# Optimization experiments

Measured on AMD Instinct MI355X. Metric: run time of the kernel, lower is better.

Reference implementation:

```python
import jax, jax.numpy as jnp
import numpy as np

B = 8192   # batch of trajectories
T = 32     # time points
H = 256    # hidden_dim
NL = 4     # num_layers
EPS = 1e-5 # LayerNorm eps (torch default)


def setup_inputs() -> dict:
    key = jax.random.key(0)
    ks = jax.random.split(key, 8)
    # xavier-ish scales (gain 0.5 for hidden, 0.1 for output, per _init_weights)
    s0 = 0.5 * np.sqrt(2.0 / (6 + H))
    sh = 0.5 * np.sqrt(2.0 / (H + H))
    so = 0.1 * np.sqrt(2.0 / (H + 3))
    return {
        "y0": jax.random.normal(ks[0], (B, 3), dtype=jnp.float32),
        "t_span": jnp.arange(T, dtype=jnp.float32) * 0.01,
        "params": jax.random.uniform(ks[1], (B, 3), dtype=jnp.float32),  # [Omega, Delta, gamma] > 0
        "W0": jax.random.normal(ks[2], (6, H), dtype=jnp.float32) * s0,
        "b0": jnp.zeros((H,), dtype=jnp.float32),
        "Wh": jax.random.normal(ks[3], (NL - 1, H, H), dtype=jnp.float32) * sh,
        "bh": jnp.zeros((NL - 1, H), dtype=jnp.float32),
        "ln_g": jnp.ones((NL, H), dtype=jnp.float32),
        "ln_b": jnp.zeros((NL, H), dtype=jnp.float32),
        "Wout": jax.random.normal(ks[4], (H, 3), dtype=jnp.float32) * so,
        "bout": jnp.zeros((3,), dtype=jnp.float32),
        "gate": jnp.float32(0.5),
    }


def _layernorm(h, g, b):
    mu = jnp.mean(h, axis=-1, keepdims=True)
    var = jnp.mean(jnp.square(h - mu), axis=-1, keepdims=True)
    return (h - mu) * jax.lax.rsqrt(var + EPS) * g + b


def reference(y0, t_span, params, W0, b0, Wh, bh, ln_g, ln_b, Wout, bout, gate):
    def correction_net(y, p):
        # input: concat([u,v,w, Omega,Delta,gamma]) -> (B, 6)
        h = jnp.concatenate([y, p], axis=-1) @ W0 + b0
        h = jax.nn.silu(_layernorm(h, ln_g[0], ln_b[0]))
        for i in range(NL - 1):
            h = jax.nn.silu(_layernorm(h @ Wh[i] + bh[i], ln_g[i + 1], ln_b[i + 1]))
        return h @ Wout + bout  # (B, 3)

    def bloch_rhs_incomplete(y, p):
        u, v, w = y[:, 0:1], y[:, 1:2], y[:, 2:3]
        Om, ga = p[:, 0:1], p[:, 2:3]
        du = -ga * u
        dv = -ga * v - Om * w
        dw = -2.0 * ga * (w + 1.0) + Om * v
        return jnp.concatenate([du, dv, dw], axis=-1)

    def f_total(y):
        return bloch_rhs_incomplete(y, params) + gate * correction_net(y, params)

    def rk4_step(y, dt):
        k1 = f_total(y)
        k2 = f_total(y + 0.5 * dt * k1)
        k3 = f_total(y + 0.5 * dt * k2)
        k4 = f_total(y + dt * k3)
        y_new = y + (dt / 6.0) * (k1 + 2.0 * k2 + 2.0 * k3 + k4)
        return y_new, y_new

    dts = jnp.diff(t_span)              # (T-1,)
    _, ys = jax.lax.scan(rk4_step, y0, dts)
    return jnp.concatenate([y0[None], ys], axis=0)  # (T, B, 3)
```

## Files before the change

kernel.cpp:

```cpp
#include <hip/hip_runtime.h>

typedef unsigned short u16;
typedef short v8s   __attribute__((ext_vector_type(8)));
typedef float f32x4 __attribute__((ext_vector_type(4)));
typedef float f32x2 __attribute__((ext_vector_type(2)));

#define H_ 256
#define B_ 8192
#define NSTEP 31
#define NTHREADS 512
#define NBLOCKS 256
#define AROW 264

#define MFMA16(a,b,c) __builtin_amdgcn_mfma_f32_16x16x32_bf16(a,b,c,0,0,0)

#define DPP_QP_XOR1 0xB1
#define DPP_QP_XOR2 0x4E
#define DPP_ROR4    0x124
#define DPP_ROR8    0x128

template<int CTRL>
__device__ __forceinline__ float dpp_add(float v){
  return v + __int_as_float(
      __builtin_amdgcn_update_dpp(0, __float_as_int(v), CTRL, 0xF, 0xF, true));
}

__device__ __forceinline__ u16 f2bf_rne(float f){
  unsigned u = __float_as_uint(f);
  u += 0x7fffu + ((u >> 16) & 1u);
  return (u16)(u >> 16);
}
__device__ __forceinline__ u16 f2bf_trunc(float f){
  return (u16)(__float_as_uint(f) >> 16);
}

#define WS_W0   0
#define WS_W1   8192
#define WS_W23  73728
#define WS_WO   204800
#define WS_TOT  205824

__global__ void prep_kernel(const float* __restrict__ W0,
                            const float* __restrict__ b0,
                            const float* __restrict__ Wh,
                            const float* __restrict__ Wout,
                            u16* __restrict__ ws){
  int i = blockIdx.x * 256 + threadIdx.x;
  if (i < 8192){
    int q = i >> 11, n = (i >> 3) & 255, j = i & 7;
    int k = q*8 + j;
    float v = (k < 6) ? W0[k*H_ + n] : ((k == 6) ? b0[n] : 0.f);
    ws[i] = f2bf_rne(v);
  } else if (i < 73728){
    int r = i - 8192;
    int n = r >> 8, k = r & 255;
    ws[i] = f2bf_rne(Wh[k*H_ + n]);
  } else if (i < 204800){
    int r = i - 73728;
    int l = r >> 16, r2 = r & 65535;
    int kc = r2 >> 13, r3 = r2 & 8191;
    int q = r3 >> 11, n = (r3 >> 3) & 255, j = r3 & 7;
    int k = kc*32 + q*8 + j;
    ws[i] = f2bf_rne(Wh[(1 + l)*H_*H_ + k*H_ + n]);
  } else if (i < WS_TOT){
    int r = i - 204800;
    int kc = r >> 7, q = (r >> 5) & 3, nn = (r >> 3) & 3, j = r & 7;
    int k = kc*32 + q*8 + j;
    ws[i] = f2bf_rne(nn < 3 ? Wout[k*3 + nn] : 0.f);
  }
}

#define PWROW 10
#define OFF_A      0
#define OFF_W1     16896
#define OFF_WOUT   152064
#define OFF_PART   154112
#define OFF_MR     156672
#define OFF_NET    156928
#define OFF_YCUR   157440
#define OFF_YSUM   157952
#define OFF_YSTG   158464
#define OFF_P      158976
#define OFF_DTS    159488
#define LDS_TOTAL  159616

__global__ __launch_bounds__(NTHREADS, 2)
void pinode_kernel(const float* __restrict__ y0g, const float* __restrict__ t_span,
                   const float* __restrict__ params, const float* __restrict__ bhg,
                   const float* __restrict__ ln_gg, const float* __restrict__ ln_bg,
                   const float* __restrict__ boutg, const float* __restrict__ gatep,
                   const u16* __restrict__ ws, float* __restrict__ out)
{
  extern __shared__ char smem[];
  u16*   A    = (u16*)(smem + OFF_A);
  u16*   W1   = (u16*)(smem + OFF_W1);
  u16*   WO   = (u16*)(smem + OFF_WOUT);
  float* part = (float*)(smem + OFF_PART);
  float* mrs  = (float*)(smem + OFF_MR);
  float* net  = (float*)(smem + OFF_NET);
  float* ycur = (float*)(smem + OFF_YCUR);
  float* ysum = (float*)(smem + OFF_YSUM);
  float* ystg = (float*)(smem + OFF_YSTG);
  float* pL   = (float*)(smem + OFF_P);
  float* dts  = (float*)(smem + OFF_DTS);

  const int tid = threadIdx.x;
  const int wave = tid >> 6;
  const int lane = tid & 63;
  const int q    = lane >> 4;
  const int c15  = lane & 15;
  const int colbase = wave * 32;
  const int s0 = blockIdx.x * 32;

  for (int idx = tid; idx < 8192; idx += NTHREADS){
    int n = idx >> 5, ch = idx & 31;
    *(v8s*)(W1 + n*AROW + ch*8) = *(const v8s*)(ws + WS_W1 + n*256 + ch*8);
  }
  if (tid < 128)
    *(v8s*)(WO + tid*8) = *(const v8s*)(ws + WS_WO + tid*8);
  if (tid < 96){
    int s = tid & 31, c = tid >> 5;
    float y = y0g[(s0+s)*3 + c];
    ycur[s*4+c] = y; ystg[s*4+c] = y;
    pL[s*4+c]   = params[(s0+s)*3 + c];
    out[(s0+s)*3 + c] = y;
  }
  if (tid < NSTEP) dts[tid] = t_span[tid+1] - t_span[tid];

  v8s wf[2][8][2];
#pragma unroll
  for (int l = 0; l < 2; ++l)
#pragma unroll
    for (int kc = 0; kc < 8; ++kc)
#pragma unroll
      for (int nt = 0; nt < 2; ++nt)
        wf[l][kc][nt] = *(const v8s*)(ws + WS_W23 +
            (((l*8 + kc)*4 + q)*256 + colbase + nt*16 + c15)*8);

  v8s w0f[2];
#pragma unroll
  for (int nt = 0; nt < 2; ++nt)
    w0f[nt] = *(const v8s*)(ws + WS_W0 + (q*256 + colbase + nt*16 + c15)*8);

  float lng[4][2], lnb[4][2], bia[4][2];
#pragma unroll
  for (int l = 0; l < 4; ++l)
#pragma unroll
    for (int nt = 0; nt < 2; ++nt){
      int col = colbase + nt*16 + c15;
      lng[l][nt] = ln_gg[l*H_ + col];
      lnb[l][nt] = ln_bg[l*H_ + col];
      bia[l][nt] = (l == 0) ? 0.f : bhg[(l-1)*H_ + col];
    }
  const float gate = gatep[0];
  const float bo0 = boutg[0], bo1 = boutg[1], bo2 = boutg[2];
  const f32x4 fzero = {0.f, 0.f, 0.f, 0.f};

  const u16* pa  = A + c15*AROW + q*8;
  const u16* pw  = W1 + (colbase + c15)*AROW + q*8;
  u16* pstA = A + (q*4)*AROW + colbase + c15;

  __syncthreads();

  {
    int s = tid >> 4, pr = tid & 15;
    int e0 = pr*2, e1 = e0 + 1;
    float x0 = (e0 < 3) ? ystg[s*4+e0] : ((e0 < 6) ? pL[s*4+e0-3] : (e0 == 6 ? 1.f : 0.f));
    float x1 = (e1 < 3) ? ystg[s*4+e1] : ((e1 < 6) ? pL[s*4+e1-3] : (e1 == 6 ? 1.f : 0.f));
    unsigned pk = (unsigned)f2bf_rne(x0) | ((unsigned)f2bf_rne(x1) << 16);
    *(unsigned*)(A + s*AROW + e0) = pk;
  }
  __syncthreads();

  auto ln_silu = [&](f32x4 (&acc)[2][2], int li){
    float rs[2][4], rq[2][4];
#pragma unroll
    for (int mt = 0; mt < 2; ++mt)
#pragma unroll
      for (int r = 0; r < 4; ++r){
        float a0 = acc[mt][0][r], a1 = acc[mt][1][r];
        rs[mt][r] = a0 + a1;
        rq[mt][r] = a0*a0 + a1*a1;
      }
#pragma unroll
    for (int mt = 0; mt < 2; ++mt)
#pragma unroll
      for (int r = 0; r < 4; ++r){
        float s = rs[mt][r], qq = rq[mt][r];
        s = dpp_add<DPP_QP_XOR1>(s);  qq = dpp_add<DPP_QP_XOR1>(qq);
        s = dpp_add<DPP_QP_XOR2>(s);  qq = dpp_add<DPP_QP_XOR2>(qq);
        s = dpp_add<DPP_ROR4>(s);     qq = dpp_add<DPP_ROR4>(qq);
        s = dpp_add<DPP_ROR8>(s);     qq = dpp_add<DPP_ROR8>(qq);
        rs[mt][r] = s; rq[mt][r] = qq;
      }
    if (c15 == 0){
#pragma unroll
      for (int mt = 0; mt < 2; ++mt)
#pragma unroll
        for (int r = 0; r < 4; ++r){
          int row = mt*16 + q*4 + r;
          f32x2 v; v.x = rs[mt][r]; v.y = rq[mt][r];
          *(f32x2*)(part + (row*PWROW + wave)*2) = v;
        }
    }
    __syncthreads();
    if (tid < 32){
      const f32x4* pp = (const f32x4*)(part + tid*PWROW*2);
      f32x4 p0 = pp[0], p1 = pp[1], p2 = pp[2], p3 = pp[3];
      float S = p0[0]+p0[2]+p1[0]+p1[2]+p2[0]+p2[2]+p3[0]+p3[2];
      float Q = p0[1]+p0[3]+p1[1]+p1[3]+p2[1]+p2[3]+p3[1]+p3[3];
      float mean = S * (1.f/256.f);
      float var  = Q * (1.f/256.f) - mean*mean;
      float rstd = rsqrtf(var + 1e-5f);
      f32x2 mr; mr.x = rstd; mr.y = -mean*rstd;
      *(f32x2*)(mrs + tid*2) = mr;
    }
    __syncthreads();
#pragma unroll
    for (int mt = 0; mt < 2; ++mt)
#pragma unroll
      for (int r = 0; r < 4; ++r){
        int row = mt*16 + q*4 + r;
        f32x2 mr = *(const f32x2*)(mrs + row*2);
#pragma unroll
        for (int nt = 0; nt < 2; ++nt){
          float t  = acc[mt][nt][r] * mr.x + mr.y;
          float v  = t * lng[li][nt] + lnb[li][nt];
          float e  = __builtin_amdgcn_exp2f(v * -1.44269504f);
          float sv = v * __builtin_amdgcn_rcpf(1.f + e);
          pstA[(mt*16 + r)*AROW + nt*16] = f2bf_trunc(sv);
        }
      }
    __syncthreads();
  };

#pragma unroll 1
  for (int step = 0; step < NSTEP; ++step){
    float dt = dts[step];
#pragma unroll 1
    for (int stage = 0; stage < 4; ++stage){
      f32x4 acc[2][2];

#pragma unroll
      for (int mt = 0; mt < 2; ++mt)
#pragma unroll
        for (int nt = 0; nt < 2; ++nt) acc[mt][nt] = fzero;
      {
        v8s a0 = *(const v8s*)(pa);
        v8s a1 = *(const v8s*)(pa + 16*AROW);
        acc[0][0] = MFMA16(a0, w0f[0], acc[0][0]);
        acc[0][1] = MFMA16(a0, w0f[1], acc[0][1]);
        acc[1][0] = MFMA16(a1, w0f[0], acc[1][0]);
        acc[1][1] = MFMA16(a1, w0f[1], acc[1][1]);
      }
      ln_silu(acc, 0);

#pragma unroll
      for (int mt = 0; mt < 2; ++mt)
#pragma unroll
        for (int nt = 0; nt < 2; ++nt) acc[mt][nt] = fzero;
#pragma unroll
      for (int kc = 0; kc < 8; ++kc){
        v8s a0 = *(const v8s*)(pa + kc*32);
        v8s a1 = *(const v8s*)(pa + 16*AROW + kc*32);
        v8s bb0 = *(const v8s*)(pw + kc*32);
        v8s bb1 = *(const v8s*)(pw + 16*AROW + kc*32);
        acc[0][0] = MFMA16(a0, bb0, acc[0][0]);
        acc[0][1] = MFMA16(a0, bb1, acc[0][1]);
        acc[1][0] = MFMA16(a1, bb0, acc[1][0]);
        acc[1][1] = MFMA16(a1, bb1, acc[1][1]);
      }
#pragma unroll
      for (int mt = 0; mt < 2; ++mt)
#pragma unroll
        for (int nt = 0; nt < 2; ++nt)
#pragma unroll
          for (int r = 0; r < 4; ++r) acc[mt][nt][r] += bia[1][nt];
      ln_silu(acc, 1);

#pragma unroll
      for (int l = 0; l < 2; ++l){
#pragma unroll
        for (int mt = 0; mt < 2; ++mt)
#pragma unroll
          for (int nt = 0; nt < 2; ++nt) acc[mt][nt] = fzero;
#pragma unroll
        for (int kc = 0; kc < 8; ++kc){
          v8s a0 = *(const v8s*)(pa + kc*32);
          v8s a1 = *(const v8s*)(pa + 16*AROW + kc*32);
          acc[0][0] = MFMA16(a0, wf[l][kc][0], acc[0][0]);
          acc[0][1] = MFMA16(a0, wf[l][kc][1], acc[0][1]);
          acc[1][0] = MFMA16(a1, wf[l][kc][0], acc[1][0]);
          acc[1][1] = MFMA16(a1, wf[l][kc][1], acc[1][1]);
        }
#pragma unroll
        for (int mt = 0; mt < 2; ++mt)
#pragma unroll
          for (int nt = 0; nt < 2; ++nt)
#pragma unroll
            for (int r = 0; r < 4; ++r) acc[mt][nt][r] += bia[2+l][nt];
        ln_silu(acc, 2+l);
      }

      if (wave < 2){
        f32x4 ao = fzero;
        int nn = c15 < 3 ? c15 : 3;
#pragma unroll
        for (int kc = 0; kc < 8; ++kc){
          v8s a = *(const v8s*)(A + (wave*16 + c15)*AROW + kc*32 + q*8);
          v8s b = *(const v8s*)(WO + ((kc*4 + q)*4 + nn)*8);
          ao = MFMA16(a, b, ao);
        }
        if (c15 < 3){
#pragma unroll
          for (int r = 0; r < 4; ++r)
            net[(wave*16 + q*4 + r)*4 + c15] = ao[r];
        }
      }
      __syncthreads();

      if (tid < 32){
        int s = tid;
        float u = ystg[s*4+0], v = ystg[s*4+1], w = ystg[s*4+2];
        float Om = pL[s*4+0], ga = pL[s*4+2];
        float kk[3];
        kk[0] = -ga*u                      + gate*(net[s*4+0] + bo0);
        kk[1] = -ga*v - Om*w               + gate*(net[s*4+1] + bo1);
        kk[2] = -2.f*ga*(w + 1.f) + Om*v   + gate*(net[s*4+2] + bo2);
#pragma unroll
        for (int c = 0; c < 3; ++c){
          float yc = ycur[s*4+c];
          float k  = kk[c];
          float ys;
          if (stage == 3){
            float accw = ysum[s*4+c] + dt*(1.f/6.f)*k;
            ycur[s*4+c] = accw;
            ys = accw;
            out[(step+1)*(B_*3) + (s0+s)*3 + c] = accw;
          } else {
            float accw = (stage == 0) ? (yc + dt*(1.f/6.f)*k)
                                      : (ysum[s*4+c] + dt*(1.f/3.f)*k);
            ysum[s*4+c] = accw;
            ys = yc + ((stage == 2) ? dt : 0.5f*dt)*k;
          }
          ystg[s*4+c] = ys;
          A[s*AROW + c] = f2bf_rne(ys);
        }
      }
      __syncthreads();
    }
  }
}

extern "C" void kernel_launch(void* const* d_in, const int* in_sizes, int n_in,
                              void* d_out, int out_size, void* d_ws, size_t ws_size,
                              hipStream_t stream) {
  const float* y0     = (const float*)d_in[0];
  const float* t_span = (const float*)d_in[1];
  const float* params = (const float*)d_in[2];
  const float* W0     = (const float*)d_in[3];
  const float* b0     = (const float*)d_in[4];
  const float* Wh     = (const float*)d_in[5];
  const float* bh     = (const float*)d_in[6];
  const float* ln_g   = (const float*)d_in[7];
  const float* ln_b   = (const float*)d_in[8];
  const float* Wout   = (const float*)d_in[9];
  const float* bout   = (const float*)d_in[10];
  const float* gate   = (const float*)d_in[11];
  float* out = (float*)d_out;
  u16* ws = (u16*)d_ws;

  prep_kernel<<<WS_TOT/256, 256, 0, stream>>>(W0, b0, Wh, Wout, ws);

  hipFuncSetAttribute(reinterpret_cast<const void*>(pinode_kernel),
                      hipFuncAttributeMaxDynamicSharedMemorySize, LDS_TOTAL);
  pinode_kernel<<<NBLOCKS, NTHREADS, LDS_TOTAL, stream>>>(
      y0, t_span, params, bh, ln_g, ln_b, bout, gate, ws, out);
}
```

Baseline: 1.167 ms.

## Software-pipeline two 16-row groups through layers with atomic LayerNorm stats

Splits the 32-sample tile into two 16-row groups and interleaves them, so one group's matmul overlaps the other group's LayerNorm/SiLU. Row statistics are accumulated with LDS atomicAdd into double-buffered stat slots instead of per-wave partials plus a separate reduce pass. This cuts barriers per layer from three to one. The output projection and RK4 update are fused into per-wave work, removing the net buffer and the tid<32 serial stage. The cost is more atomics and more complex sequencing that depends on careful zeroing of the stat slots.

```diff
diff --git a/kernel.cpp b/kernel.cpp
--- a/kernel.cpp
+++ b/kernel.cpp
@@ -70,19 +70,16 @@
   }
 }
 
-#define PWROW 10
 #define OFF_A      0
 #define OFF_W1     16896
 #define OFF_WOUT   152064
-#define OFF_PART   154112
-#define OFF_MR     156672
-#define OFF_NET    156928
-#define OFF_YCUR   157440
-#define OFF_YSUM   157952
-#define OFF_YSTG   158464
-#define OFF_P      158976
-#define OFF_DTS    159488
-#define LDS_TOTAL  159616
+#define OFF_STAT   154112
+#define OFF_YCUR   154624
+#define OFF_YSUM   155136
+#define OFF_YSTG   155648
+#define OFF_P      156160
+#define OFF_DTS    156672
+#define LDS_TOTAL  156800
 
 __global__ __launch_bounds__(NTHREADS, 2)
 void pinode_kernel(const float* __restrict__ y0g, const float* __restrict__ t_span,
@@ -95,9 +92,7 @@
   u16*   A    = (u16*)(smem + OFF_A);
   u16*   W1   = (u16*)(smem + OFF_W1);
   u16*   WO   = (u16*)(smem + OFF_WOUT);
-  float* part = (float*)(smem + OFF_PART);
-  float* mrs  = (float*)(smem + OFF_MR);
-  float* net  = (float*)(smem + OFF_NET);
+  float* stat = (float*)(smem + OFF_STAT);
   float* ycur = (float*)(smem + OFF_YCUR);
   float* ysum = (float*)(smem + OFF_YSUM);
   float* ystg = (float*)(smem + OFF_YSTG);
@@ -109,6 +104,7 @@
   const int lane = tid & 63;
   const int q    = lane >> 4;
   const int c15  = lane & 15;
+  const int nn   = (c15 < 3) ? c15 : 3;
   const int colbase = wave * 32;
   const int s0 = blockIdx.x * 32;
 
@@ -126,6 +122,7 @@
     out[(s0+s)*3 + c] = y;
   }
   if (tid < NSTEP) dts[tid] = t_span[tid+1] - t_span[tid];
+  if (tid < 128) stat[tid] = 0.f;
 
   v8s wf[2][8][2];
 #pragma unroll
@@ -158,7 +155,6 @@
 
   const u16* pa  = A + c15*AROW + q*8;
   const u16* pw  = W1 + (colbase + c15)*AROW + q*8;
-  u16* pstA = A + (q*4)*AROW + colbase + c15;
 
   __syncthreads();
 
@@ -172,183 +168,182 @@
   }
   __syncthreads();
 
-  auto ln_silu = [&](f32x4 (&acc)[2][2], int li){
-    float rs[2][4], rq[2][4];
-#pragma unroll
-    for (int mt = 0; mt < 2; ++mt)
+
+  auto zstat = [&](int g, int par){
+    if (tid < 16)
+      *(f32x2*)(stat + ((g*2 + par)*16 + tid)*2) = (f32x2){0.f, 0.f};
+  };
+
+  auto mm0 = [&](f32x4 (&acc)[2], int g){
+    v8s a = *(const v8s*)(pa + g*16*AROW);
+    acc[0] = MFMA16(a, w0f[0], fzero);
+    acc[1] = MFMA16(a, w0f[1], fzero);
+  };
+
+  auto mm1 = [&](f32x4 (&acc)[2], int g){
+    float b0i = bia[1][0], b1i = bia[1][1];
+    acc[0] = (f32x4){b0i,b0i,b0i,b0i};
+    acc[1] = (f32x4){b1i,b1i,b1i,b1i};
+    const u16* pag = pa + g*16*AROW;
+#pragma unroll
+    for (int kc = 0; kc < 8; ++kc){
+      v8s a   = *(const v8s*)(pag + kc*32);
+      v8s bb0 = *(const v8s*)(pw + kc*32);
+      v8s bb1 = *(const v8s*)(pw + 16*AROW + kc*32);
+      acc[0] = MFMA16(a, bb0, acc[0]);
+      acc[1] = MFMA16(a, bb1, acc[1]);
+    }
+  };
+
+  auto mmr = [&](f32x4 (&acc)[2], int g, int lw){
+    float b0i = bia[2+lw][0], b1i = bia[2+lw][1];
+    acc[0] = (f32x4){b0i,b0i,b0i,b0i};
+    acc[1] = (f32x4){b1i,b1i,b1i,b1i};
+    const u16* pag = pa + g*16*AROW;
+#pragma unroll
+    for (int kc = 0; kc < 8; ++kc){
+      v8s a = *(const v8s*)(pag + kc*32);
+      acc[0] = MFMA16(a, wf[lw][kc][0], acc[0]);
+      acc[1] = MFMA16(a, wf[lw][kc][1], acc[1]);
+    }
+  };
+
+  auto red_write = [&](f32x4 (&acc)[2], int g, int par){
+    float rs[4], rq[4];
+#pragma unroll
+    for (int r = 0; r < 4; ++r){
+      float a0 = acc[0][r], a1 = acc[1][r];
+      rs[r] = a0 + a1;
+      rq[r] = a0*a0 + a1*a1;
+    }
+#pragma unroll
+    for (int r = 0; r < 4; ++r){
+      float s = rs[r], qq = rq[r];
+      s = dpp_add<DPP_QP_XOR1>(s);  qq = dpp_add<DPP_QP_XOR1>(qq);
+      s = dpp_add<DPP_QP_XOR2>(s);  qq = dpp_add<DPP_QP_XOR2>(qq);
+      s = dpp_add<DPP_ROR4>(s);     qq = dpp_add<DPP_ROR4>(qq);
+      s = dpp_add<DPP_ROR8>(s);     qq = dpp_add<DPP_ROR8>(qq);
+      rs[r] = s; rq[r] = qq;
+    }
+    if (c15 == 0){
+      float* bp = stat + ((g*2 + par)*16 + q*4)*2;
 #pragma unroll
       for (int r = 0; r < 4; ++r){
-        float a0 = acc[mt][0][r], a1 = acc[mt][1][r];
-        rs[mt][r] = a0 + a1;
-        rq[mt][r] = a0*a0 + a1*a1;
+        atomicAdd(bp + r*2 + 0, rs[r]);
+        atomicAdd(bp + r*2 + 1, rq[r]);
       }
-#pragma unroll
-    for (int mt = 0; mt < 2; ++mt)
+    }
+  };
+
+  auto finrm = [&](f32x4 (&acc)[2], int g, int li){
+    const int par = li & 1;
+    const float* bp = stat + ((g*2 + par)*16 + q*4)*2;
+    f32x4 st01 = *(const f32x4*)(bp);
+    f32x4 st23 = *(const f32x4*)(bp + 4);
+    float S[4] = {st01[0], st01[2], st23[0], st23[2]};
+    float Q[4] = {st01[1], st01[3], st23[1], st23[3]};
+    u16* pst = A + (g*16 + q*4)*AROW + colbase + c15;
+#pragma unroll
+    for (int r = 0; r < 4; ++r){
+      float mean = S[r] * (1.f/256.f);
+      float var  = Q[r] * (1.f/256.f) - mean*mean;
+      float rstd = rsqrtf(var + 1e-5f);
+      float mb   = -mean * rstd;
+#pragma unroll
+      for (int nt = 0; nt < 2; ++nt){
+        float t  = acc[nt][r] * rstd + mb;
+        float v  = t * lng[li][nt] + lnb[li][nt];
+        float e  = __builtin_amdgcn_exp2f(v * -1.44269504f);
+        float sv = v * __builtin_amdgcn_rcpf(1.f + e);
+        pst[r*AROW + nt*16] = f2bf_trunc(sv);
+      }
+    }
+  };
+
+  auto outrk4 = [&](int g, int step, int stage){
+    f32x4 ao = fzero;
+    const u16* pao = A + (g*16 + c15)*AROW + q*8;
+#pragma unroll
+    for (int kc = 0; kc < 8; ++kc){
+      v8s a = *(const v8s*)(pao + kc*32);
+      v8s b = *(const v8s*)(WO + ((kc*4 + q)*4 + nn)*8);
+      ao = MFMA16(a, b, ao);
+    }
+    float dt = dts[step];
+    if (c15 == 3){
 #pragma unroll
       for (int r = 0; r < 4; ++r){
-        float s = rs[mt][r], qq = rq[mt][r];
-        s = dpp_add<DPP_QP_XOR1>(s);  qq = dpp_add<DPP_QP_XOR1>(qq);
-        s = dpp_add<DPP_QP_XOR2>(s);  qq = dpp_add<DPP_QP_XOR2>(qq);
-        s = dpp_add<DPP_ROR4>(s);     qq = dpp_add<DPP_ROR4>(qq);
-        s = dpp_add<DPP_ROR8>(s);     qq = dpp_add<DPP_ROR8>(qq);
-        rs[mt][r] = s; rq[mt][r] = qq;
+        int s = g*16 + q*4 + r;
+        *(unsigned*)(A + s*AROW + 6) = 0x00003F80u;
       }
-    if (c15 == 0){
-#pragma unroll
-      for (int mt = 0; mt < 2; ++mt)
-#pragma unroll
-        for (int r = 0; r < 4; ++r){
-          int row = mt*16 + q*4 + r;
-          f32x2 v; v.x = rs[mt][r]; v.y = rq[mt][r];
-          *(f32x2*)(part + (row*PWROW + wave)*2) = v;
+    }
+    if (c15 < 3){
+      const int c = c15;
+      const float boc = (c == 0) ? bo0 : ((c == 1) ? bo1 : bo2);
+#pragma unroll
+      for (int r = 0; r < 4; ++r){
+        int s = g*16 + q*4 + r;
+        float Om = pL[s*4+0], ga = pL[s*4+2];
+        float yi  = ystg[s*4+c];
+        float oth = ystg[s*4 + ((c == 1) ? 2 : 1)];
+        float kA = (c == 2) ? (Om*oth - 2.f*ga*(yi + 1.f))
+                            : (-ga*yi - ((c == 1) ? Om*oth : 0.f));
+        float kk = kA + gate*(ao[r] + boc);
+        float yc = ycur[s*4+c];
+        if (stage == 3){
+          float acw = ysum[s*4+c] + dt*(1.f/6.f)*kk;
+          ycur[s*4+c] = acw;
+          ystg[s*4+c] = acw;
+          A[s*AROW + c] = f2bf_rne(acw);
+          out[(step+1)*(B_*3) + (s0+s)*3 + c] = acw;
+        } else {
+          float acw = (stage == 0) ? (yc + dt*(1.f/6.f)*kk)
+                                   : (ysum[s*4+c] + dt*(1.f/3.f)*kk);
+          ysum[s*4+c] = acw;
+          float ysn = yc + ((stage == 2) ? dt : 0.5f*dt)*kk;
+          ystg[s*4+c] = ysn;
+          A[s*AROW + c] = f2bf_rne(ysn);
         }
-    }
-    __syncthreads();
-    if (tid < 32){
-      const f32x4* pp = (const f32x4*)(part + tid*PWROW*2);
-      f32x4 p0 = pp[0], p1 = pp[1], p2 = pp[2], p3 = pp[3];
-      float S = p0[0]+p0[2]+p1[0]+p1[2]+p2[0]+p2[2]+p3[0]+p3[2];
-      float Q = p0[1]+p0[3]+p1[1]+p1[3]+p2[1]+p2[3]+p3[1]+p3[3];
-      float mean = S * (1.f/256.f);
-      float var  = Q * (1.f/256.f) - mean*mean;
-      float rstd = rsqrtf(var + 1e-5f);
-      f32x2 mr; mr.x = rstd; mr.y = -mean*rstd;
-      *(f32x2*)(mrs + tid*2) = mr;
-    }
-    __syncthreads();
-#pragma unroll
-    for (int mt = 0; mt < 2; ++mt)
-#pragma unroll
-      for (int r = 0; r < 4; ++r){
-        int row = mt*16 + q*4 + r;
-        f32x2 mr = *(const f32x2*)(mrs + row*2);
-#pragma unroll
-        for (int nt = 0; nt < 2; ++nt){
-          float t  = acc[mt][nt][r] * mr.x + mr.y;
-          float v  = t * lng[li][nt] + lnb[li][nt];
-          float e  = __builtin_amdgcn_exp2f(v * -1.44269504f);
-          float sv = v * __builtin_amdgcn_rcpf(1.f + e);
-          pstA[(mt*16 + r)*AROW + nt*16] = f2bf_trunc(sv);
-        }
+        A[s*AROW + 3 + c] = f2bf_rne(pL[s*4+c]);
       }
-    __syncthreads();
-  };
+    }
+  };
+
+  f32x4 accA[2], accB[2];
+
+  mm0(accA, 0); red_write(accA, 0, 0); zstat(0, 1);
+  __syncthreads();
 
 #pragma unroll 1
-  for (int step = 0; step < NSTEP; ++step){
-    float dt = dts[step];
-#pragma unroll 1
-    for (int stage = 0; stage < 4; ++stage){
-      f32x4 acc[2][2];
-
-#pragma unroll
-      for (int mt = 0; mt < 2; ++mt)
-#pragma unroll
-        for (int nt = 0; nt < 2; ++nt) acc[mt][nt] = fzero;
-      {
-        v8s a0 = *(const v8s*)(pa);
-        v8s a1 = *(const v8s*)(pa + 16*AROW);
-        acc[0][0] = MFMA16(a0, w0f[0], acc[0][0]);
-        acc[0][1] = MFMA16(a0, w0f[1], acc[0][1]);
-        acc[1][0] = MFMA16(a1, w0f[0], acc[1][0]);
-        acc[1][1] = MFMA16(a1, w0f[1], acc[1][1]);
-      }
-      ln_silu(acc, 0);
-
-#pragma unroll
-      for (int mt = 0; mt < 2; ++mt)
-#pragma unroll
-        for (int nt = 0; nt < 2; ++nt) acc[mt][nt] = fzero;
-#pragma unroll
-      for (int kc = 0; kc < 8; ++kc){
-        v8s a0 = *(const v8s*)(pa + kc*32);
-        v8s a1 = *(const v8s*)(pa + 16*AROW + kc*32);
-        v8s bb0 = *(const v8s*)(pw + kc*32);
-        v8s bb1 = *(const v8s*)(pw + 16*AROW + kc*32);
-        acc[0][0] = MFMA16(a0, bb0, acc[0][0]);
-        acc[0][1] = MFMA16(a0, bb1, acc[0][1]);
-        acc[1][0] = MFMA16(a1, bb0, acc[1][0]);
-        acc[1][1] = MFMA16(a1, bb1, acc[1][1]);
-      }
-#pragma unroll
-      for (int mt = 0; mt < 2; ++mt)
-#pragma unroll
-        for (int nt = 0; nt < 2; ++nt)
-#pragma unroll
-          for (int r = 0; r < 4; ++r) acc[mt][nt][r] += bia[1][nt];
-      ln_silu(acc, 1);
-
-#pragma unroll
-      for (int l = 0; l < 2; ++l){
-#pragma unroll
-        for (int mt = 0; mt < 2; ++mt)
-#pragma unroll
-          for (int nt = 0; nt < 2; ++nt) acc[mt][nt] = fzero;
-#pragma unroll
-        for (int kc = 0; kc < 8; ++kc){
-          v8s a0 = *(const v8s*)(pa + kc*32);
-          v8s a1 = *(const v8s*)(pa + 16*AROW + kc*32);
-          acc[0][0] = MFMA16(a0, wf[l][kc][0], acc[0][0]);
-          acc[0][1] = MFMA16(a0, wf[l][kc][1], acc[0][1]);
-          acc[1][0] = MFMA16(a1, wf[l][kc][0], acc[1][0]);
-          acc[1][1] = MFMA16(a1, wf[l][kc][1], acc[1][1]);
-        }
-#pragma unroll
-        for (int mt = 0; mt < 2; ++mt)
-#pragma unroll
-          for (int nt = 0; nt < 2; ++nt)
-#pragma unroll
-            for (int r = 0; r < 4; ++r) acc[mt][nt][r] += bia[2+l][nt];
-        ln_silu(acc, 2+l);
-      }
-
-      if (wave < 2){
-        f32x4 ao = fzero;
-        int nn = c15 < 3 ? c15 : 3;
-#pragma unroll
-        for (int kc = 0; kc < 8; ++kc){
-          v8s a = *(const v8s*)(A + (wave*16 + c15)*AROW + kc*32 + q*8);
-          v8s b = *(const v8s*)(WO + ((kc*4 + q)*4 + nn)*8);
-          ao = MFMA16(a, b, ao);
-        }
-        if (c15 < 3){
-#pragma unroll
-          for (int r = 0; r < 4; ++r)
-            net[(wave*16 + q*4 + r)*4 + c15] = ao[r];
-        }
-      }
-      __syncthreads();
-
-      if (tid < 32){
-        int s = tid;
-        float u = ystg[s*4+0], v = ystg[s*4+1], w = ystg[s*4+2];
-        float Om = pL[s*4+0], ga = pL[s*4+2];
-        float kk[3];
-        kk[0] = -ga*u                      + gate*(net[s*4+0] + bo0);
-        kk[1] = -ga*v - Om*w               + gate*(net[s*4+1] + bo1);
-        kk[2] = -2.f*ga*(w + 1.f) + Om*v   + gate*(net[s*4+2] + bo2);
-#pragma unroll
-        for (int c = 0; c < 3; ++c){
-          float yc = ycur[s*4+c];
-          float k  = kk[c];
-          float ys;
-          if (stage == 3){
-            float accw = ysum[s*4+c] + dt*(1.f/6.f)*k;
-            ycur[s*4+c] = accw;
-            ys = accw;
-            out[(step+1)*(B_*3) + (s0+s)*3 + c] = accw;
-          } else {
-            float accw = (stage == 0) ? (yc + dt*(1.f/6.f)*k)
-                                      : (ysum[s*4+c] + dt*(1.f/3.f)*k);
-            ysum[s*4+c] = accw;
-            ys = yc + ((stage == 2) ? dt : 0.5f*dt)*k;
-          }
-          ystg[s*4+c] = ys;
-          A[s*AROW + c] = f2bf_rne(ys);
-        }
-      }
-      __syncthreads();
-    }
+  for (int it = 0; it < NSTEP*4; ++it){
+    const int step = it >> 2, stage = it & 3;
+
+    mm0(accB, 1); finrm(accA, 0, 0); red_write(accB, 1, 0); zstat(1, 1);
+    __syncthreads();
+
+    mm1(accA, 0); finrm(accB, 1, 0); red_write(accA, 0, 1); zstat(0, 0);
+    __syncthreads();
+    mm1(accB, 1); finrm(accA, 0, 1); red_write(accB, 1, 1); zstat(1, 0);
+    __syncthreads();
+
+    mmr(accA, 0, 0); finrm(accB, 1, 1); red_write(accA, 0, 0); zstat(0, 1);
+    __syncthreads();
+    mmr(accB, 1, 0); finrm(accA, 0, 2); red_write(accB, 1, 0); zstat(1, 1);
+    __syncthreads();
+
+    mmr(accA, 0, 1); finrm(accB, 1, 2); red_write(accA, 0, 1); zstat(0, 0);
+    __syncthreads();
+    mmr(accB, 1, 1); finrm(accA, 0, 3); red_write(accB, 1, 1); zstat(1, 0);
+    __syncthreads();
+
+    finrm(accB, 1, 3);
+    if (wave == 0) outrk4(0, step, stage);
+    __syncthreads();
+
+    if (it + 1 < NSTEP*4){ mm0(accA, 0); }
+    if (wave == 1) outrk4(1, step, stage);
+    if (it + 1 < NSTEP*4){ red_write(accA, 0, 0); zstat(0, 1); }
+    __syncthreads();
   }
 }
 
```

New measurement: 1.708 ms. 1.46x slower.

## Split hidden columns across sixteen waves using 1024-thread blocks

Applied to the files above, without the earlier changes.

Doubles the block to 1024 threads so each of 16 waves owns 16 output columns instead of 32. This halves per-wave MFMA work and register-resident weight fragments, and aims to give each CU more waves to hide LDS and MFMA latency. The LayerNorm partial-sum buffer grows to hold 16 wave partials, and the final reducer sums eight vector loads. Each stage now also rewrites the parameter and bias-one columns of the activation tile. In exchange, B-fragment reuse per wave drops and each barrier has more waves to synchronise.

```diff
diff --git a/kernel.cpp b/kernel.cpp
--- a/kernel.cpp
+++ b/kernel.cpp
@@ -8,7 +8,8 @@
 #define H_ 256
 #define B_ 8192
 #define NSTEP 31
-#define NTHREADS 512
+#define NTHREADS 1024
+#define NWAVES 16
 #define NBLOCKS 256
 #define AROW 264
 
@@ -70,21 +71,21 @@
   }
 }
 
-#define PWROW 10
+#define PSTRIDE 18
 #define OFF_A      0
 #define OFF_W1     16896
 #define OFF_WOUT   152064
 #define OFF_PART   154112
-#define OFF_MR     156672
-#define OFF_NET    156928
-#define OFF_YCUR   157440
-#define OFF_YSUM   157952
-#define OFF_YSTG   158464
-#define OFF_P      158976
-#define OFF_DTS    159488
-#define LDS_TOTAL  159616
-
-__global__ __launch_bounds__(NTHREADS, 2)
+#define OFF_NET    158720
+#define OFF_MR     159232
+#define OFF_YCUR   159488
+#define OFF_YSUM   160000
+#define OFF_YSTG   160512
+#define OFF_P      161024
+#define OFF_DTS    161536
+#define LDS_TOTAL  161664
+
+__global__ __launch_bounds__(NTHREADS, 4)
 void pinode_kernel(const float* __restrict__ y0g, const float* __restrict__ t_span,
                    const float* __restrict__ params, const float* __restrict__ bhg,
                    const float* __restrict__ ln_gg, const float* __restrict__ ln_bg,
@@ -96,8 +97,8 @@
   u16*   W1   = (u16*)(smem + OFF_W1);
   u16*   WO   = (u16*)(smem + OFF_WOUT);
   float* part = (float*)(smem + OFF_PART);
+  float* net  = (float*)(smem + OFF_NET);
   float* mrs  = (float*)(smem + OFF_MR);
-  float* net  = (float*)(smem + OFF_NET);
   float* ycur = (float*)(smem + OFF_YCUR);
   float* ysum = (float*)(smem + OFF_YSUM);
   float* ystg = (float*)(smem + OFF_YSTG);
@@ -109,7 +110,7 @@
   const int lane = tid & 63;
   const int q    = lane >> 4;
   const int c15  = lane & 15;
-  const int colbase = wave * 32;
+  const int colbase = wave * 16;
   const int s0 = blockIdx.x * 32;
 
   for (int idx = tid; idx < 8192; idx += NTHREADS){
@@ -127,31 +128,24 @@
   }
   if (tid < NSTEP) dts[tid] = t_span[tid+1] - t_span[tid];
 
-  v8s wf[2][8][2];
+  v8s wf[2][8];
 #pragma unroll
   for (int l = 0; l < 2; ++l)
 #pragma unroll
     for (int kc = 0; kc < 8; ++kc)
-#pragma unroll
-      for (int nt = 0; nt < 2; ++nt)
-        wf[l][kc][nt] = *(const v8s*)(ws + WS_W23 +
-            (((l*8 + kc)*4 + q)*256 + colbase + nt*16 + c15)*8);
-
-  v8s w0f[2];
-#pragma unroll
-  for (int nt = 0; nt < 2; ++nt)
-    w0f[nt] = *(const v8s*)(ws + WS_W0 + (q*256 + colbase + nt*16 + c15)*8);
-
-  float lng[4][2], lnb[4][2], bia[4][2];
-#pragma unroll
-  for (int l = 0; l < 4; ++l)
-#pragma unroll
-    for (int nt = 0; nt < 2; ++nt){
-      int col = colbase + nt*16 + c15;
-      lng[l][nt] = ln_gg[l*H_ + col];
-      lnb[l][nt] = ln_bg[l*H_ + col];
-      bia[l][nt] = (l == 0) ? 0.f : bhg[(l-1)*H_ + col];
-    }
+      wf[l][kc] = *(const v8s*)(ws + WS_W23 +
+          (((l*8 + kc)*4 + q)*256 + colbase + c15)*8);
+
+  v8s w0f = *(const v8s*)(ws + WS_W0 + (q*256 + colbase + c15)*8);
+
+  float lng[4], lnb[4], bia[4];
+#pragma unroll
+  for (int l = 0; l < 4; ++l){
+    int col = colbase + c15;
+    lng[l] = ln_gg[l*H_ + col];
+    lnb[l] = ln_bg[l*H_ + col];
+    bia[l] = (l == 0) ? 0.f : bhg[(l-1)*H_ + col];
+  }
   const float gate = gatep[0];
   const float bo0 = boutg[0], bo1 = boutg[1], bo2 = boutg[2];
   const f32x4 fzero = {0.f, 0.f, 0.f, 0.f};
@@ -162,7 +156,7 @@
 
   __syncthreads();
 
-  {
+  if (tid < 512){
     int s = tid >> 4, pr = tid & 15;
     int e0 = pr*2, e1 = e0 + 1;
     float x0 = (e0 < 3) ? ystg[s*4+e0] : ((e0 < 6) ? pL[s*4+e0-3] : (e0 == 6 ? 1.f : 0.f));
@@ -172,15 +166,15 @@
   }
   __syncthreads();
 
-  auto ln_silu = [&](f32x4 (&acc)[2][2], int li){
+  auto ln_silu = [&](f32x4 (&acc)[2], int li){
     float rs[2][4], rq[2][4];
 #pragma unroll
     for (int mt = 0; mt < 2; ++mt)
 #pragma unroll
       for (int r = 0; r < 4; ++r){
-        float a0 = acc[mt][0][r], a1 = acc[mt][1][r];
-        rs[mt][r] = a0 + a1;
-        rq[mt][r] = a0*a0 + a1*a1;
+        float a0 = acc[mt][r];
+        rs[mt][r] = a0;
+        rq[mt][r] = a0*a0;
       }
 #pragma unroll
     for (int mt = 0; mt < 2; ++mt)
@@ -200,15 +194,19 @@
         for (int r = 0; r < 4; ++r){
           int row = mt*16 + q*4 + r;
           f32x2 v; v.x = rs[mt][r]; v.y = rq[mt][r];
-          *(f32x2*)(part + (row*PWROW + wave)*2) = v;
+          *(f32x2*)(part + (row*PSTRIDE + wave)*2) = v;
         }
     }
     __syncthreads();
     if (tid < 32){
-      const f32x4* pp = (const f32x4*)(part + tid*PWROW*2);
-      f32x4 p0 = pp[0], p1 = pp[1], p2 = pp[2], p3 = pp[3];
-      float S = p0[0]+p0[2]+p1[0]+p1[2]+p2[0]+p2[2]+p3[0]+p3[2];
-      float Q = p0[1]+p0[3]+p1[1]+p1[3]+p2[1]+p2[3]+p3[1]+p3[3];
+      const f32x4* pp = (const f32x4*)(part + tid*PSTRIDE*2);
+      float S = 0.f, Q = 0.f;
+#pragma unroll
+      for (int k = 0; k < 8; ++k){
+        f32x4 p = pp[k];
+        S += p[0] + p[2];
+        Q += p[1] + p[3];
+      }
       float mean = S * (1.f/256.f);
       float var  = Q * (1.f/256.f) - mean*mean;
       float rstd = rsqrtf(var + 1e-5f);
@@ -222,14 +220,11 @@
       for (int r = 0; r < 4; ++r){
         int row = mt*16 + q*4 + r;
         f32x2 mr = *(const f32x2*)(mrs + row*2);
-#pragma unroll
-        for (int nt = 0; nt < 2; ++nt){
-          float t  = acc[mt][nt][r] * mr.x + mr.y;
-          float v  = t * lng[li][nt] + lnb[li][nt];
-          float e  = __builtin_amdgcn_exp2f(v * -1.44269504f);
-          float sv = v * __builtin_amdgcn_rcpf(1.f + e);
-          pstA[(mt*16 + r)*AROW + nt*16] = f2bf_trunc(sv);
-        }
+        float t  = acc[mt][r] * mr.x + mr.y;
+        float v  = t * lng[li] + lnb[li];
+        float e  = __builtin_amdgcn_exp2f(v * -1.44269504f);
+        float sv = v * __builtin_amdgcn_rcpf(1.f + e);
+        pstA[(mt*16 + r)*AROW] = f2bf_trunc(sv);
       }
     __syncthreads();
   };
@@ -239,66 +234,45 @@
     float dt = dts[step];
 #pragma unroll 1
     for (int stage = 0; stage < 4; ++stage){
-      f32x4 acc[2][2];
-
-#pragma unroll
-      for (int mt = 0; mt < 2; ++mt)
-#pragma unroll
-        for (int nt = 0; nt < 2; ++nt) acc[mt][nt] = fzero;
+      f32x4 acc[2];
+
       {
         v8s a0 = *(const v8s*)(pa);
         v8s a1 = *(const v8s*)(pa + 16*AROW);
-        acc[0][0] = MFMA16(a0, w0f[0], acc[0][0]);
-        acc[0][1] = MFMA16(a0, w0f[1], acc[0][1]);
-        acc[1][0] = MFMA16(a1, w0f[0], acc[1][0]);
-        acc[1][1] = MFMA16(a1, w0f[1], acc[1][1]);
+        acc[0] = MFMA16(a0, w0f, fzero);
+        acc[1] = MFMA16(a1, w0f, fzero);
       }
       ln_silu(acc, 0);
 
-#pragma unroll
-      for (int mt = 0; mt < 2; ++mt)
-#pragma unroll
-        for (int nt = 0; nt < 2; ++nt) acc[mt][nt] = fzero;
+      acc[0] = fzero; acc[1] = fzero;
 #pragma unroll
       for (int kc = 0; kc < 8; ++kc){
         v8s a0 = *(const v8s*)(pa + kc*32);
         v8s a1 = *(const v8s*)(pa + 16*AROW + kc*32);
-        v8s bb0 = *(const v8s*)(pw + kc*32);
-        v8s bb1 = *(const v8s*)(pw + 16*AROW + kc*32);
-        acc[0][0] = MFMA16(a0, bb0, acc[0][0]);
-        acc[0][1] = MFMA16(a0, bb1, acc[0][1]);
-        acc[1][0] = MFMA16(a1, bb0, acc[1][0]);
-        acc[1][1] = MFMA16(a1, bb1, acc[1][1]);
+        v8s bb = *(const v8s*)(pw + kc*32);
+        acc[0] = MFMA16(a0, bb, acc[0]);
+        acc[1] = MFMA16(a1, bb, acc[1]);
       }
 #pragma unroll
       for (int mt = 0; mt < 2; ++mt)
 #pragma unroll
-        for (int nt = 0; nt < 2; ++nt)
-#pragma unroll
-          for (int r = 0; r < 4; ++r) acc[mt][nt][r] += bia[1][nt];
+        for (int r = 0; r < 4; ++r) acc[mt][r] += bia[1];
       ln_silu(acc, 1);
 
 #pragma unroll
       for (int l = 0; l < 2; ++l){
-#pragma unroll
-        for (int mt = 0; mt < 2; ++mt)
-#pragma unroll
-          for (int nt = 0; nt < 2; ++nt) acc[mt][nt] = fzero;
+        acc[0] = fzero; acc[1] = fzero;
 #pragma unroll
         for (int kc = 0; kc < 8; ++kc){
           v8s a0 = *(const v8s*)(pa + kc*32);
           v8s a1 = *(const v8s*)(pa + 16*AROW + kc*32);
-          acc[0][0] = MFMA16(a0, wf[l][kc][0], acc[0][0]);
-          acc[0][1] = MFMA16(a0, wf[l][kc][1], acc[0][1]);
-          acc[1][0] = MFMA16(a1, wf[l][kc][0], acc[1][0]);
-          acc[1][1] = MFMA16(a1, wf[l][kc][1], acc[1][1]);
+          acc[0] = MFMA16(a0, wf[l][kc], acc[0]);
+          acc[1] = MFMA16(a1, wf[l][kc], acc[1]);
         }
 #pragma unroll
         for (int mt = 0; mt < 2; ++mt)
 #pragma unroll
-          for (int nt = 0; nt < 2; ++nt)
-#pragma unroll
-            for (int r = 0; r < 4; ++r) acc[mt][nt][r] += bia[2+l][nt];
+          for (int r = 0; r < 4; ++r) acc[mt][r] += bia[2+l];
         ln_silu(acc, 2+l);
       }
 
@@ -345,7 +319,9 @@
           }
           ystg[s*4+c] = ys;
           A[s*AROW + c] = f2bf_rne(ys);
-        }
+          A[s*AROW + 3 + c] = f2bf_rne(pL[s*4+c]);
+        }
+        *(unsigned*)(A + s*AROW + 6) = 0x00003F80u;
       }
       __syncthreads();
     }
```

New measurement: 1.793 ms. 1.54x slower.

## Split rows across two wave groups with 1024 threads and stream hidden weights from global

Applied to the files above, without the earlier changes.

Doubles the block to 1024 threads. Each group of 8 waves now owns 16 of the block's 32 rows instead of every wave computing both M-tiles, which halves per-wave MFMA work and the accumulator registers. The layer-2/3 weights are no longer held in registers; they are reloaded from global memory (L2) in chunks of four K-slices. This frees VGPRs so that 1024 threads fit per block. The stage update now rewrites the params and bias-one columns of A each stage. The costs are extra global/L2 traffic on every layer and possibly lower occupancy, since LDS use already limits residency.

```diff
diff --git a/kernel.cpp b/kernel.cpp
--- a/kernel.cpp
+++ b/kernel.cpp
@@ -8,7 +8,7 @@
 #define H_ 256
 #define B_ 8192
 #define NSTEP 31
-#define NTHREADS 512
+#define NTHREADS 1024
 #define NBLOCKS 256
 #define AROW 264
 
@@ -84,7 +84,7 @@
 #define OFF_DTS    159488
 #define LDS_TOTAL  159616
 
-__global__ __launch_bounds__(NTHREADS, 2)
+__global__ __launch_bounds__(NTHREADS)
 void pinode_kernel(const float* __restrict__ y0g, const float* __restrict__ t_span,
                    const float* __restrict__ params, const float* __restrict__ bhg,
                    const float* __restrict__ ln_gg, const float* __restrict__ ln_bg,
@@ -109,7 +109,9 @@
   const int lane = tid & 63;
   const int q    = lane >> 4;
   const int c15  = lane & 15;
-  const int colbase = wave * 32;
+  const int g    = wave >> 3;
+  const int w    = wave & 7;
+  const int colbase = w * 32;
   const int s0 = blockIdx.x * 32;
 
   for (int idx = tid; idx < 8192; idx += NTHREADS){
@@ -127,20 +129,12 @@
   }
   if (tid < NSTEP) dts[tid] = t_span[tid+1] - t_span[tid];
 
-  v8s wf[2][8][2];
-#pragma unroll
-  for (int l = 0; l < 2; ++l)
-#pragma unroll
-    for (int kc = 0; kc < 8; ++kc)
-#pragma unroll
-      for (int nt = 0; nt < 2; ++nt)
-        wf[l][kc][nt] = *(const v8s*)(ws + WS_W23 +
-            (((l*8 + kc)*4 + q)*256 + colbase + nt*16 + c15)*8);
-
   v8s w0f[2];
 #pragma unroll
   for (int nt = 0; nt < 2; ++nt)
     w0f[nt] = *(const v8s*)(ws + WS_W0 + (q*256 + colbase + nt*16 + c15)*8);
+
+  const u16* pW23 = ws + WS_W23 + (q*256 + colbase + c15)*8;
 
   float lng[4][2], lnb[4][2], bia[4][2];
 #pragma unroll
@@ -156,13 +150,13 @@
   const float bo0 = boutg[0], bo1 = boutg[1], bo2 = boutg[2];
   const f32x4 fzero = {0.f, 0.f, 0.f, 0.f};
 
-  const u16* pa  = A + c15*AROW + q*8;
+  const u16* pa  = A + (g*16 + c15)*AROW + q*8;
   const u16* pw  = W1 + (colbase + c15)*AROW + q*8;
-  u16* pstA = A + (q*4)*AROW + colbase + c15;
+  u16* pstA = A + (g*16 + q*4)*AROW + colbase + c15;
 
   __syncthreads();
 
-  {
+  if (tid < 512){
     int s = tid >> 4, pr = tid & 15;
     int e0 = pr*2, e1 = e0 + 1;
     float x0 = (e0 < 3) ? ystg[s*4+e0] : ((e0 < 6) ? pL[s*4+e0-3] : (e0 == 6 ? 1.f : 0.f));
@@ -172,36 +166,30 @@
   }
   __syncthreads();
 
-  auto ln_silu = [&](f32x4 (&acc)[2][2], int li){
-    float rs[2][4], rq[2][4];
-#pragma unroll
-    for (int mt = 0; mt < 2; ++mt)
+  auto ln_silu = [&](f32x4 (&acc)[2], int li){
+    float rs[4], rq[4];
+#pragma unroll
+    for (int r = 0; r < 4; ++r){
+      float a0 = acc[0][r], a1 = acc[1][r];
+      rs[r] = a0 + a1;
+      rq[r] = a0*a0 + a1*a1;
+    }
+#pragma unroll
+    for (int r = 0; r < 4; ++r){
+      float s = rs[r], qq = rq[r];
+      s = dpp_add<DPP_QP_XOR1>(s);  qq = dpp_add<DPP_QP_XOR1>(qq);
+      s = dpp_add<DPP_QP_XOR2>(s);  qq = dpp_add<DPP_QP_XOR2>(qq);
+      s = dpp_add<DPP_ROR4>(s);     qq = dpp_add<DPP_ROR4>(qq);
+      s = dpp_add<DPP_ROR8>(s);     qq = dpp_add<DPP_ROR8>(qq);
+      rs[r] = s; rq[r] = qq;
+    }
+    if (c15 == 0){
 #pragma unroll
       for (int r = 0; r < 4; ++r){
-        float a0 = acc[mt][0][r], a1 = acc[mt][1][r];
-        rs[mt][r] = a0 + a1;
-        rq[mt][r] = a0*a0 + a1*a1;
-      }
-#pragma unroll
-    for (int mt = 0; mt < 2; ++mt)
-#pragma unroll
-      for (int r = 0; r < 4; ++r){
-        float s = rs[mt][r], qq = rq[mt][r];
-        s = dpp_add<DPP_QP_XOR1>(s);  qq = dpp_add<DPP_QP_XOR1>(qq);
-        s = dpp_add<DPP_QP_XOR2>(s);  qq = dpp_add<DPP_QP_XOR2>(qq);
-        s = dpp_add<DPP_ROR4>(s);     qq = dpp_add<DPP_ROR4>(qq);
-        s = dpp_add<DPP_ROR8>(s);     qq = dpp_add<DPP_ROR8>(qq);
-        rs[mt][r] = s; rq[mt][r] = qq;
-      }
-    if (c15 == 0){
-#pragma unroll
-      for (int mt = 0; mt < 2; ++mt)
-#pragma unroll
-        for (int r = 0; r < 4; ++r){
-          int row = mt*16 + q*4 + r;
-          f32x2 v; v.x = rs[mt][r]; v.y = rq[mt][r];
-          *(f32x2*)(part + (row*PWROW + wave)*2) = v;
-        }
+        int row = g*16 + q*4 + r;
+        f32x2 v; v.x = rs[r]; v.y = rq[r];
+        *(f32x2*)(part + (row*PWROW + w)*2) = v;
+      }
     }
     __syncthreads();
     if (tid < 32){
@@ -217,20 +205,18 @@
     }
     __syncthreads();
 #pragma unroll
-    for (int mt = 0; mt < 2; ++mt)
-#pragma unroll
-      for (int r = 0; r < 4; ++r){
-        int row = mt*16 + q*4 + r;
-        f32x2 mr = *(const f32x2*)(mrs + row*2);
-#pragma unroll
-        for (int nt = 0; nt < 2; ++nt){
-          float t  = acc[mt][nt][r] * mr.x + mr.y;
-          float v  = t * lng[li][nt] + lnb[li][nt];
-          float e  = __builtin_amdgcn_exp2f(v * -1.44269504f);
-          float sv = v * __builtin_amdgcn_rcpf(1.f + e);
-          pstA[(mt*16 + r)*AROW + nt*16] = f2bf_trunc(sv);
-        }
-      }
+    for (int r = 0; r < 4; ++r){
+      int row = g*16 + q*4 + r;
+      f32x2 mr = *(const f32x2*)(mrs + row*2);
+#pragma unroll
+      for (int nt = 0; nt < 2; ++nt){
+        float t  = acc[nt][r] * mr.x + mr.y;
+        float v  = t * lng[li][nt] + lnb[li][nt];
+        float e  = __builtin_amdgcn_exp2f(v * -1.44269504f);
+        float sv = v * __builtin_amdgcn_rcpf(1.f + e);
+        pstA[r*AROW + nt*16] = f2bf_trunc(sv);
+      }
+    }
     __syncthreads();
   };
 
@@ -239,94 +225,81 @@
     float dt = dts[step];
 #pragma unroll 1
     for (int stage = 0; stage < 4; ++stage){
-      f32x4 acc[2][2];
-
-#pragma unroll
-      for (int mt = 0; mt < 2; ++mt)
-#pragma unroll
-        for (int nt = 0; nt < 2; ++nt) acc[mt][nt] = fzero;
+      f32x4 acc[2];
+
       {
-        v8s a0 = *(const v8s*)(pa);
-        v8s a1 = *(const v8s*)(pa + 16*AROW);
-        acc[0][0] = MFMA16(a0, w0f[0], acc[0][0]);
-        acc[0][1] = MFMA16(a0, w0f[1], acc[0][1]);
-        acc[1][0] = MFMA16(a1, w0f[0], acc[1][0]);
-        acc[1][1] = MFMA16(a1, w0f[1], acc[1][1]);
+        v8s a = *(const v8s*)(pa);
+        acc[0] = MFMA16(a, w0f[0], fzero);
+        acc[1] = MFMA16(a, w0f[1], fzero);
       }
       ln_silu(acc, 0);
 
-#pragma unroll
-      for (int mt = 0; mt < 2; ++mt)
-#pragma unroll
-        for (int nt = 0; nt < 2; ++nt) acc[mt][nt] = fzero;
+      acc[0] = fzero; acc[1] = fzero;
 #pragma unroll
       for (int kc = 0; kc < 8; ++kc){
-        v8s a0 = *(const v8s*)(pa + kc*32);
-        v8s a1 = *(const v8s*)(pa + 16*AROW + kc*32);
-        v8s bb0 = *(const v8s*)(pw + kc*32);
-        v8s bb1 = *(const v8s*)(pw + 16*AROW + kc*32);
-        acc[0][0] = MFMA16(a0, bb0, acc[0][0]);
-        acc[0][1] = MFMA16(a0, bb1, acc[0][1]);
-        acc[1][0] = MFMA16(a1, bb0, acc[1][0]);
-        acc[1][1] = MFMA16(a1, bb1, acc[1][1]);
-      }
-#pragma unroll
-      for (int mt = 0; mt < 2; ++mt)
+        v8s a  = *(const v8s*)(pa + kc*32);
+        v8s b0 = *(const v8s*)(pw + kc*32);
+        v8s b1 = *(const v8s*)(pw + 16*AROW + kc*32);
+        acc[0] = MFMA16(a, b0, acc[0]);
+        acc[1] = MFMA16(a, b1, acc[1]);
+      }
+#pragma unroll
+      for (int nt = 0; nt < 2; ++nt)
+#pragma unroll
+        for (int r = 0; r < 4; ++r) acc[nt][r] += bia[1][nt];
+      ln_silu(acc, 1);
+
+#pragma unroll
+      for (int l = 0; l < 2; ++l){
+        acc[0] = fzero; acc[1] = fzero;
+#pragma unroll 1
+        for (int h = 0; h < 2; ++h){
+          v8s lw[4][2];
+#pragma unroll
+          for (int i = 0; i < 4; ++i){
+            int kc = l*8 + h*4 + i;
+            lw[i][0] = *(const v8s*)(pW23 + kc*8192);
+            lw[i][1] = *(const v8s*)(pW23 + kc*8192 + 128);
+          }
+#pragma unroll
+          for (int i = 0; i < 4; ++i){
+            v8s a = *(const v8s*)(pa + (h*4 + i)*32);
+            acc[0] = MFMA16(a, lw[i][0], acc[0]);
+            acc[1] = MFMA16(a, lw[i][1], acc[1]);
+          }
+        }
 #pragma unroll
         for (int nt = 0; nt < 2; ++nt)
 #pragma unroll
-          for (int r = 0; r < 4; ++r) acc[mt][nt][r] += bia[1][nt];
-      ln_silu(acc, 1);
-
-#pragma unroll
-      for (int l = 0; l < 2; ++l){
-#pragma unroll
-        for (int mt = 0; mt < 2; ++mt)
-#pragma unroll
-          for (int nt = 0; nt < 2; ++nt) acc[mt][nt] = fzero;
-#pragma unroll
-        for (int kc = 0; kc < 8; ++kc){
-          v8s a0 = *(const v8s*)(pa + kc*32);
-          v8s a1 = *(const v8s*)(pa + 16*AROW + kc*32);
-          acc[0][0] = MFMA16(a0, wf[l][kc][0], acc[0][0]);
-          acc[0][1] = MFMA16(a0, wf[l][kc][1], acc[0][1]);
-          acc[1][0] = MFMA16(a1, wf[l][kc][0], acc[1][0]);
-          acc[1][1] = MFMA16(a1, wf[l][kc][1], acc[1][1]);
-        }
-#pragma unroll
-        for (int mt = 0; mt < 2; ++mt)
-#pragma unroll
-          for (int nt = 0; nt < 2; ++nt)
-#pragma unroll
-            for (int r = 0; r < 4; ++r) acc[mt][nt][r] += bia[2+l][nt];
+          for (int r = 0; r < 4; ++r) acc[nt][r] += bia[2+l][nt];
         ln_silu(acc, 2+l);
       }
 
-      if (wave < 2){
+      if (w == 0){
         f32x4 ao = fzero;
         int nn = c15 < 3 ? c15 : 3;
 #pragma unroll
         for (int kc = 0; kc < 8; ++kc){
-          v8s a = *(const v8s*)(A + (wave*16 + c15)*AROW + kc*32 + q*8);
+          v8s a = *(const v8s*)(pa + kc*32);
           v8s b = *(const v8s*)(WO + ((kc*4 + q)*4 + nn)*8);
           ao = MFMA16(a, b, ao);
         }
         if (c15 < 3){
 #pragma unroll
           for (int r = 0; r < 4; ++r)
-            net[(wave*16 + q*4 + r)*4 + c15] = ao[r];
+            net[(g*16 + q*4 + r)*4 + c15] = ao[r];
         }
       }
       __syncthreads();
 
       if (tid < 32){
         int s = tid;
-        float u = ystg[s*4+0], v = ystg[s*4+1], w = ystg[s*4+2];
+        float u = ystg[s*4+0], v = ystg[s*4+1], ww = ystg[s*4+2];
         float Om = pL[s*4+0], ga = pL[s*4+2];
         float kk[3];
-        kk[0] = -ga*u                      + gate*(net[s*4+0] + bo0);
-        kk[1] = -ga*v - Om*w               + gate*(net[s*4+1] + bo1);
-        kk[2] = -2.f*ga*(w + 1.f) + Om*v   + gate*(net[s*4+2] + bo2);
+        kk[0] = -ga*u                       + gate*(net[s*4+0] + bo0);
+        kk[1] = -ga*v - Om*ww               + gate*(net[s*4+1] + bo1);
+        kk[2] = -2.f*ga*(ww + 1.f) + Om*v   + gate*(net[s*4+2] + bo2);
 #pragma unroll
         for (int c = 0; c < 3; ++c){
           float yc = ycur[s*4+c];
@@ -345,7 +318,9 @@
           }
           ystg[s*4+c] = ys;
           A[s*AROW + c] = f2bf_rne(ys);
+          A[s*AROW + 3 + c] = f2bf_rne(pL[s*4+c]);
         }
+        *(unsigned*)(A + s*AROW + 6) = 0x00003F80u;
       }
       __syncthreads();
     }
```

After: 1.404 ms. +20.3%, slower.
